# Optimization experiments

Measured on AMD Instinct MI355X. Metric: run time of the kernel, lower is better.

Reference implementation:

```python
import jax, jax.numpy as jnp
import numpy as np

PHASE_BINS = 100
EPS = 1e-10
W_AMP = 0.5
W_PHASE = 0.5


def setup_inputs() -> dict:
    key = jax.random.key(0)
    kA, kB = jax.random.split(key)
    A = jax.random.normal(kA, (64, 2, 512, 512), dtype=jnp.float32)
    B = jax.random.normal(kB, (64, 2, 512, 512), dtype=jnp.float32)
    return {"A": A, "B": B}


def _to_complex(x):
    # (batch, 2, H, W) -> complex (batch, H, W)
    return jax.lax.complex(x[:, 0, :, :], x[:, 1, :, :])


def _kl(p, q):
    # torch.sum over the last TWO dims (faithful: for 2D [batch,bins] phase
    # histograms this collapses to a scalar, like the original code).
    return jnp.sum(p * jnp.log((p + EPS) / (q + EPS)), axis=(-2, -1))


def _phase_hist_density(phase, edges):
    # phase: (batch, H, W). torch.histogram with density=True.
    b = phase.shape[0]
    n = phase.shape[1] * phase.shape[2]
    flat = phase.reshape(b, n)
    # rightmost edge inclusive in last bin (torch semantics)
    idx = jnp.clip(jnp.searchsorted(edges, flat, side="right") - 1, 0, PHASE_BINS - 1)
    counts = jax.vmap(
        lambda i: jnp.zeros((PHASE_BINS,), jnp.float32).at[i].add(1.0)
    )(idx)
    width = edges[1:] - edges[:-1]  # (bins,)
    return counts / (jnp.float32(n) * width)  # density


def reference(A, B):
    edges = jnp.linspace(-np.pi, np.pi, PHASE_BINS + 1, dtype=jnp.float32)
    Ac = _to_complex(A)
    Bc = _to_complex(B)

    # amplitude KL, shape (batch,)
    Aa = jnp.abs(Ac)
    Ba = jnp.abs(Bc)
    P = Aa / (jnp.sum(Aa, axis=(-2, -1), keepdims=True) + EPS)
    Q = Ba / (jnp.sum(Ba, axis=(-2, -1), keepdims=True) + EPS)
    amp_loss = _kl(P, Q)

    # phase KL (scalar, summed over batch per original dim=(-2,-1) on 2D hist)
    Pp = _phase_hist_density(jnp.angle(Ac), edges)
    Qp = _phase_hist_density(jnp.angle(Bc), edges)
    Pp = Pp / (jnp.sum(Pp, axis=-1, keepdims=True) + EPS)
    Qp = Qp / (jnp.sum(Qp, axis=-1, keepdims=True) + EPS)
    phase_loss = _kl(Pp, Qp)

    return W_AMP * amp_loss + W_PHASE * phase_loss
```

## Files before the change

### kernel.cpp

```cpp
#include <hip/hip_runtime.h>
#include <math.h>

#define PHASE_BINS 100
#define EPSF 1e-10f
#define HW 262144
#define BATCH 64
#define BPB 32
#define CHUNK (HW / BPB)
#define THREADS 256
#define GROUPS (CHUNK / (THREADS * 4))

__device__ __forceinline__ float wave_reduce_sum(float v) {
    #pragma unroll
    for (int off = 32; off > 0; off >>= 1) v += __shfl_down(v, off, 64);
    return v;
}

__device__ __forceinline__ int phase_bin(float y, float x) {
    const float PI_F = 3.14159265358979323846f;
    float ax = fabsf(x), ay = fabsf(y);
    float mx = fmaxf(ax, ay), mn = fminf(ax, ay);
    float r  = mn * __builtin_amdgcn_rcpf(mx);
    float rr = (r - 1.0f) * __builtin_amdgcn_rcpf(r + 1.0f);
    bool big = r > 0.4142135624f;
    float z = big ? rr : r;
    float s = z * z;
    float p = fmaf(fmaf(fmaf(8.05374449538e-2f, s, -1.38776856032e-1f), s,
                        1.99777106478e-1f), s, -3.33329491539e-1f);
    float th = fmaf(z * s, p, z);
    th += big ? 0.78539816340f : 0.0f;
    th = (ay > ax) ? 1.57079632679f - th : th;
    th = (x < 0.0f) ? PI_F - th : th;
    th = (y < 0.0f) ? -th : th;
    int bin = (int)((th + PI_F) * 15.9154943092f);
    return min(max(bin, 0), PHASE_BINS - 1);
}

__global__ __launch_bounds__(THREADS) void pass1_kernel(
    const float* __restrict__ A, const float* __restrict__ B,
    float* __restrict__ SA, float* __restrict__ SB, float* __restrict__ Tacc,
    unsigned int* __restrict__ histA, unsigned int* __restrict__ histB)
{
    __shared__ unsigned int h[2][4][PHASE_BINS];
    const int wave = threadIdx.x >> 6;
    const int lane = threadIdx.x & 63;

    for (int i = threadIdx.x; i < 2 * 4 * PHASE_BINS; i += THREADS)
        ((unsigned int*)h)[i] = 0u;
    __syncthreads();

    unsigned int* __restrict__ hA = &h[0][wave][0];
    unsigned int* __restrict__ hB = &h[1][wave][0];

    const int b   = blockIdx.x / BPB;
    const int blk = blockIdx.x % BPB;
    const size_t base = (size_t)b * (2 * HW);
    const float* Ar = A + base;
    const float* Ai = Ar + HW;
    const float* Br = B + base;
    const float* Bi = Br + HW;

    float sA = 0.f, sB = 0.f, t = 0.f;

    int idx = blk * CHUNK + threadIdx.x * 4;
    float4 car = *(const float4*)(Ar + idx);
    float4 cai = *(const float4*)(Ai + idx);
    float4 cbr = *(const float4*)(Br + idx);
    float4 cbi = *(const float4*)(Bi + idx);

    #pragma unroll 1
    for (int g = 0; g < GROUPS; ++g) {
        const int nidx = idx + THREADS * 4;
        float4 nar, nai, nbr, nbi;
        if (g + 1 < GROUPS) {
            nar = *(const float4*)(Ar + nidx);
            nai = *(const float4*)(Ai + nidx);
            nbr = *(const float4*)(Br + nidx);
            nbi = *(const float4*)(Bi + nidx);
        }
        const float* arp = (const float*)&car;
        const float* aip = (const float*)&cai;
        const float* brp = (const float*)&cbr;
        const float* bip = (const float*)&cbi;
        #pragma unroll
        for (int j = 0; j < 4; ++j) {
            float arj = arp[j], aij = aip[j];
            float brj = brp[j], bij = bip[j];
            float ra2 = fmaf(arj, arj, aij * aij);
            float rb2 = fmaf(brj, brj, bij * bij);
            float aa = __builtin_amdgcn_sqrtf(ra2);
            float bb = __builtin_amdgcn_sqrtf(rb2);
            sA += aa;
            sB += bb;
            float q = ra2 * __builtin_amdgcn_rcpf(rb2);
            q = fminf(fmaxf(q, 1e-37f), 1e37f);
            t = fmaf(aa * 0.34657359028f, __log2f(q), t);
            atomicAdd(hA + phase_bin(aij, arj), 1u);
            atomicAdd(hB + phase_bin(bij, brj), 1u);
        }
        car = nar; cai = nai; cbr = nbr; cbi = nbi;
        idx = nidx;
    }

    sA = wave_reduce_sum(sA);
    sB = wave_reduce_sum(sB);
    t  = wave_reduce_sum(t);
    if (lane == 0) {
        atomicAdd(&SA[b], sA);
        atomicAdd(&SB[b], sB);
        atomicAdd(&Tacc[b], t);
    }

    __syncthreads();
    if (threadIdx.x < 2 * PHASE_BINS) {
        int hi  = threadIdx.x / PHASE_BINS;
        int bin = threadIdx.x % PHASE_BINS;
        unsigned v = h[hi][0][bin] + h[hi][1][bin] + h[hi][2][bin] + h[hi][3][bin];
        unsigned int* dst = hi ? histB : histA;
        atomicAdd(&dst[b * PHASE_BINS + bin], v);
    }
}

__global__ __launch_bounds__(64) void pass2a_kernel(
    const float* __restrict__ SA, const float* __restrict__ SB,
    const float* __restrict__ T,
    const unsigned int* __restrict__ histA, const unsigned int* __restrict__ histB,
    float* __restrict__ amp, float* __restrict__ phase_total)
{
    const int b = blockIdx.x;
    const int lane = threadIdx.x;
    const float PI_F = 3.14159265358979323846f;
    const float step = (2.0f * PI_F) / PHASE_BINS;

    float d_a[2], d_b[2];
    float sum_a = 0.f, sum_b = 0.f;
    #pragma unroll
    for (int r = 0; r < 2; ++r) {
        int bin = lane + r * 64;
        float da = 0.f, db = 0.f;
        if (bin < PHASE_BINS) {
            float e0 = -PI_F + bin * step;
            float e1 = (bin == PHASE_BINS - 1) ? PI_F : (-PI_F + (bin + 1) * step);
            float w = e1 - e0;
            float denom = (float)HW * w;
            da = (float)histA[b * PHASE_BINS + bin] / denom;
            db = (float)histB[b * PHASE_BINS + bin] / denom;
        }
        d_a[r] = da; d_b[r] = db;
        sum_a += da; sum_b += db;
    }
    #pragma unroll
    for (int off = 32; off > 0; off >>= 1) {
        sum_a += __shfl_xor(sum_a, off, 64);
        sum_b += __shfl_xor(sum_b, off, 64);
    }
    float kl = 0.f;
    #pragma unroll
    for (int r = 0; r < 2; ++r) {
        int bin = lane + r * 64;
        if (bin < PHASE_BINS) {
            float p = d_a[r] / (sum_a + EPSF);
            float q = d_b[r] / (sum_b + EPSF);
            kl += p * logf((p + EPSF) / (q + EPSF));
        }
    }
    #pragma unroll
    for (int off = 32; off > 0; off >>= 1) kl += __shfl_xor(kl, off, 64);

    if (lane == 0) {
        atomicAdd(phase_total, kl);
        float sa_raw = SA[b];
        float sa = sa_raw + EPSF;
        float sb = SB[b] + EPSF;
        amp[b] = T[b] / sa + (sa_raw / sa) * logf(sb / sa);
    }
}

__global__ __launch_bounds__(64) void pass2b_kernel(
    const float* __restrict__ amp, const float* __restrict__ phase_total,
    float* __restrict__ out)
{
    int b = threadIdx.x;
    out[b] = 0.5f * amp[b] + 0.5f * phase_total[0];
}

extern "C" void kernel_launch(void* const* d_in, const int* in_sizes, int n_in,
                              void* d_out, int out_size, void* d_ws, size_t ws_size,
                              hipStream_t stream) {
    const float* A = (const float*)d_in[0];
    const float* B = (const float*)d_in[1];
    float* out = (float*)d_out;

    float* SA = (float*)d_ws;
    float* SB = SA + BATCH;
    float* T  = SB + BATCH;
    unsigned int* histA = (unsigned int*)(T + BATCH);
    unsigned int* histB = histA + BATCH * PHASE_BINS;
    float* phase_total = (float*)(histB + BATCH * PHASE_BINS);
    float* amp = phase_total + 1;

    size_t zero_bytes = (size_t)(3 * BATCH) * sizeof(float)
                      + (size_t)(2 * BATCH * PHASE_BINS) * sizeof(unsigned int)
                      + sizeof(float);
    hipMemsetAsync(d_ws, 0, zero_bytes, stream);

    pass1_kernel<<<dim3(BATCH * BPB), dim3(THREADS), 0, stream>>>(
        A, B, SA, SB, T, histA, histB);
    pass2a_kernel<<<dim3(BATCH), dim3(64), 0, stream>>>(
        SA, SB, T, histA, histB, amp, phase_total);
    pass2b_kernel<<<1, 64, 0, stream>>>(amp, phase_total, out);
}
```

Baseline: 300.5 us.

## Peel prefetch loop, use single-range atan polynomial, split log ratio, raise occupancy

Replaces the range-reduced atan (an rcp plus a select) with a higher-degree minimax polynomial on [0,1]. The amplitude log-ratio is now the difference of two log2 calls instead of an rcp and a clamp. The prefetch loop is peeled so the last iteration carries no branch, a sched_barrier keeps the next loads issued before the compute, and launch bounds request 8 blocks per CU for occupancy. This trades an rcp for a second log and more FMAs, and the new polynomial's precision near bin edges could shift histogram counts.

```diff
diff --git a/kernel.cpp b/kernel.cpp
--- a/kernel.cpp
+++ b/kernel.cpp
@@ -16,19 +16,24 @@
     return v;
 }
 
+__device__ __forceinline__ float atan01(float z) {
+    float s = z * z;
+    float p = fmaf(s, 0.0028662257f, -0.0161657367f);
+    p = fmaf(s, p, 0.0429096138f);
+    p = fmaf(s, p, -0.0752896400f);
+    p = fmaf(s, p, 0.1065626393f);
+    p = fmaf(s, p, -0.1420889944f);
+    p = fmaf(s, p, 0.1999355085f);
+    p = fmaf(s, p, -0.3333314528f);
+    return fmaf(z * s, p, z);
+}
+
 __device__ __forceinline__ int phase_bin(float y, float x) {
     const float PI_F = 3.14159265358979323846f;
     float ax = fabsf(x), ay = fabsf(y);
     float mx = fmaxf(ax, ay), mn = fminf(ax, ay);
     float r  = mn * __builtin_amdgcn_rcpf(mx);
-    float rr = (r - 1.0f) * __builtin_amdgcn_rcpf(r + 1.0f);
-    bool big = r > 0.4142135624f;
-    float z = big ? rr : r;
-    float s = z * z;
-    float p = fmaf(fmaf(fmaf(8.05374449538e-2f, s, -1.38776856032e-1f), s,
-                        1.99777106478e-1f), s, -3.33329491539e-1f);
-    float th = fmaf(z * s, p, z);
-    th += big ? 0.78539816340f : 0.0f;
+    float th = atan01(r);
     th = (ay > ax) ? 1.57079632679f - th : th;
     th = (x < 0.0f) ? PI_F - th : th;
     th = (y < 0.0f) ? -th : th;
@@ -36,7 +41,31 @@
     return min(max(bin, 0), PHASE_BINS - 1);
 }
 
-__global__ __launch_bounds__(THREADS) void pass1_kernel(
+#define PROC4(vAr, vAi, vBr, vBi)                                          \
+    {                                                                       \
+        const float* arp = (const float*)&vAr;                              \
+        const float* aip = (const float*)&vAi;                              \
+        const float* brp = (const float*)&vBr;                              \
+        const float* bip = (const float*)&vBi;                              \
+        _Pragma("unroll")                                                   \
+        for (int j = 0; j < 4; ++j) {                                       \
+            float arj = arp[j], aij = aip[j];                               \
+            float brj = brp[j], bij = bip[j];                               \
+            float ra2 = fmaf(arj, arj, aij * aij);                          \
+            float rb2 = fmaf(brj, brj, bij * bij);                          \
+            float aa = __builtin_amdgcn_sqrtf(ra2);                         \
+            float bb = __builtin_amdgcn_sqrtf(rb2);                         \
+            sA += aa;                                                       \
+            sB += bb;                                                       \
+            float la = __log2f(fmaxf(ra2, 1e-37f));                         \
+            float lb = __log2f(fmaxf(rb2, 1e-37f));                         \
+            t = fmaf(aa * 0.34657359028f, la - lb, t);                      \
+            atomicAdd(hA + phase_bin(aij, arj), 1u);                        \
+            atomicAdd(hB + phase_bin(bij, brj), 1u);                        \
+        }                                                                   \
+    }
+
+__global__ __launch_bounds__(THREADS, 8) void pass1_kernel(
     const float* __restrict__ A, const float* __restrict__ B,
     float* __restrict__ SA, float* __restrict__ SB, float* __restrict__ Tacc,
     unsigned int* __restrict__ histA, unsigned int* __restrict__ histB)
@@ -63,44 +92,23 @@
     float sA = 0.f, sB = 0.f, t = 0.f;
 
     int idx = blk * CHUNK + threadIdx.x * 4;
-    float4 car = *(const float4*)(Ar + idx);
-    float4 cai = *(const float4*)(Ai + idx);
-    float4 cbr = *(const float4*)(Br + idx);
-    float4 cbi = *(const float4*)(Bi + idx);
+    float4 cAr = *(const float4*)(Ar + idx);
+    float4 cAi = *(const float4*)(Ai + idx);
+    float4 cBr = *(const float4*)(Br + idx);
+    float4 cBi = *(const float4*)(Bi + idx);
 
     #pragma unroll 1
-    for (int g = 0; g < GROUPS; ++g) {
-        const int nidx = idx + THREADS * 4;
-        float4 nar, nai, nbr, nbi;
-        if (g + 1 < GROUPS) {
-            nar = *(const float4*)(Ar + nidx);
-            nai = *(const float4*)(Ai + nidx);
-            nbr = *(const float4*)(Br + nidx);
-            nbi = *(const float4*)(Bi + nidx);
-        }
-        const float* arp = (const float*)&car;
-        const float* aip = (const float*)&cai;
-        const float* brp = (const float*)&cbr;
-        const float* bip = (const float*)&cbi;
-        #pragma unroll
-        for (int j = 0; j < 4; ++j) {
-            float arj = arp[j], aij = aip[j];
-            float brj = brp[j], bij = bip[j];
-            float ra2 = fmaf(arj, arj, aij * aij);
-            float rb2 = fmaf(brj, brj, bij * bij);
-            float aa = __builtin_amdgcn_sqrtf(ra2);
-            float bb = __builtin_amdgcn_sqrtf(rb2);
-            sA += aa;
-            sB += bb;
-            float q = ra2 * __builtin_amdgcn_rcpf(rb2);
-            q = fminf(fmaxf(q, 1e-37f), 1e37f);
-            t = fmaf(aa * 0.34657359028f, __log2f(q), t);
-            atomicAdd(hA + phase_bin(aij, arj), 1u);
-            atomicAdd(hB + phase_bin(bij, brj), 1u);
-        }
-        car = nar; cai = nai; cbr = nbr; cbi = nbi;
-        idx = nidx;
-    }
+    for (int g = 0; g < GROUPS - 1; ++g) {
+        idx += THREADS * 4;
+        float4 nAr = *(const float4*)(Ar + idx);
+        float4 nAi = *(const float4*)(Ai + idx);
+        float4 nBr = *(const float4*)(Br + idx);
+        float4 nBi = *(const float4*)(Bi + idx);
+        __builtin_amdgcn_sched_barrier(0);
+        PROC4(cAr, cAi, cBr, cBi);
+        cAr = nAr; cAi = nAi; cBr = nBr; cBi = nBi;
+    }
+    PROC4(cAr, cAi, cBr, cBi);
 
     sA = wave_reduce_sum(sA);
     sB = wave_reduce_sum(sB);
```

Result: faster. 293.8 us (-2.2%).
